# Optimization experiments

Measured on AMD Instinct MI355X. Metric: run time of the kernel, lower is better.

## Reference

```python
import jax, jax.numpy as jnp
import numpy as np
from itertools import product

# Static config
B, H, W, C = 16, 64, 64, 256
WIN = 8            # window size (square)
SHIFT = 4          # cyclic shift
NH = 8             # heads
HD = C // NH       # head dim
N = WIN * WIN      # tokens per window
HIDDEN = 1024


def _rel_pos_index():
    coords = np.stack(np.meshgrid(np.arange(WIN), np.arange(WIN), indexing='ij'))  # (2,w,w)
    flat = coords.reshape(2, -1)                                   # (2,N)
    rel = flat[:, :, None] - flat[:, None, :]                      # (2,N,N)
    rel = rel.transpose(1, 2, 0).astype(np.int64)
    rel[..., 0] += WIN - 1
    rel[..., 1] += WIN - 1
    rel[..., 0] *= 2 * WIN - 1
    return rel.sum(-1)                                             # (N,N)


def _shift_mask():
    # additive mask (nW, N, N) with -100 across shift boundaries (generate_mask)
    img = np.zeros((H, W), dtype=np.float32)
    slices = [(slice(0, -WIN), slice(-WIN, -SHIFT), slice(-SHIFT, None))] * 2
    cnt = 0
    for sx, sy in product(*slices):
        img[sx, sy] = cnt
        cnt += 1
    mw = img.reshape(H // WIN, WIN, W // WIN, WIN).transpose(0, 2, 1, 3).reshape(-1, N)  # (nW,N)
    diff = mw[:, None, :] - mw[:, :, None]
    return np.where(diff != 0, -100.0, 0.0).astype(np.float32)     # (nW,N,N)


REL_IDX = jnp.asarray(_rel_pos_index())
MASK = jnp.asarray(_shift_mask())


def _layernorm(x, scale, bias, eps=1e-5):
    mu = jnp.mean(x, axis=-1, keepdims=True)
    var = jnp.mean(jnp.square(x - mu), axis=-1, keepdims=True)
    return (x - mu) * jax.lax.rsqrt(var + eps) * scale + bias


def setup_inputs() -> dict:
    key = jax.random.key(0)
    ks = jax.random.split(key, 8)
    s = lambda fan_in: 1.0 / np.sqrt(fan_in)
    return {
        'x': jax.random.normal(ks[0], (B, H, W, C), jnp.float32),
        'ln1_scale': jnp.ones((C,), jnp.float32),
        'ln1_bias': jnp.zeros((C,), jnp.float32),
        'qkv_w': jax.random.normal(ks[1], (3 * C, C), jnp.float32) * s(C),
        'qkv_b': jnp.zeros((3 * C,), jnp.float32),
        'proj_w': jax.random.normal(ks[2], (C, C), jnp.float32) * s(C),
        'proj_b': jnp.zeros((C,), jnp.float32),
        'rel_bias': jax.random.normal(ks[3], ((2 * WIN - 1) ** 2, NH), jnp.float32) * 0.02,
        'ln2_scale': jnp.ones((C,), jnp.float32),
        'ln2_bias': jnp.zeros((C,), jnp.float32),
        'mlp_w1': jax.random.normal(ks[4], (HIDDEN, C), jnp.float32) * s(C),
        'mlp_b1': jnp.zeros((HIDDEN,), jnp.float32),
        'mlp_w2': jax.random.normal(ks[5], (C, HIDDEN), jnp.float32) * s(HIDDEN),
        'mlp_b2': jnp.zeros((C,), jnp.float32),
    }


def reference(x, ln1_scale, ln1_bias, qkv_w, qkv_b, proj_w, proj_b, rel_bias,
              ln2_scale, ln2_bias, mlp_w1, mlp_b1, mlp_w2, mlp_b2):
    nWh, nWw = H // WIN, W // WIN
    nW = nWh * nWw

    shortcut = x
    h = _layernorm(x, ln1_scale, ln1_bias)
    # cyclic shift
    h = jnp.roll(h, shift=(-SHIFT, -SHIFT), axis=(1, 2))
    # window partition -> (B*nW, N, C)
    h = h.reshape(B, nWh, WIN, nWw, WIN, C).transpose(0, 1, 3, 2, 4, 5).reshape(B * nW, N, C)

    # qkv
    qkv = h @ qkv_w.T + qkv_b                                # (B*nW, N, 3C)
    qkv = qkv.reshape(B * nW, N, 3, NH, HD)
    q, k, v = qkv[:, :, 0], qkv[:, :, 1], qkv[:, :, 2]       # (B*nW, N, NH, HD)

    scale = 1.0 / np.sqrt(HD)
    attn = jnp.einsum('bnhd,bmhd->bhnm', q * scale, k)       # (B*nW, NH, N, N)
    attn = attn + rel_bias[REL_IDX].transpose(2, 0, 1)[None]  # rel-pos bias (NH,N,N)
    attn = attn.reshape(B, nW, NH, N, N) + MASK[None, :, None]
    attn = jax.nn.softmax(attn.reshape(B * nW, NH, N, N), axis=-1)

    out = jnp.einsum('bhnm,bmhd->bnhd', attn, v).reshape(B * nW, N, C)
    out = out @ proj_w.T + proj_b

    # window reverse + reverse shift
    out = out.reshape(B, nWh, nWw, WIN, WIN, C).transpose(0, 1, 3, 2, 4, 5).reshape(B, H, W, C)
    out = jnp.roll(out, shift=(SHIFT, SHIFT), axis=(1, 2))

    x = shortcut + out
    # MLP
    h2 = _layernorm(x, ln2_scale, ln2_bias)
    h2 = jax.nn.gelu(h2 @ mlp_w1.T + mlp_b1, approximate=False) @ mlp_w2.T + mlp_b2
    return x + h2
```

## Files before the change

### kernel.cpp

```cpp
#include <hip/hip_runtime.h>
#include <hip/hip_bf16.h>
#include <math.h>

#define AS1 __attribute__((address_space(1)))
#define AS3 __attribute__((address_space(3)))

typedef __bf16  bf16x8 __attribute__((ext_vector_type(8)));
typedef float   f32x4  __attribute__((ext_vector_type(4)));
typedef __hip_bfloat16 bf16;

__device__ __forceinline__ void gload_lds16(const void* g, void* l) {
  __builtin_amdgcn_global_load_lds((const AS1 void*)g, (AS3 void*)l, 16, 0, 0);
}

__global__ __launch_bounds__(256) void k_conv_weights(
    const float* __restrict__ qkvw, const float* __restrict__ projw,
    const float* __restrict__ w1, const float* __restrict__ w2,
    bf16* __restrict__ dst)
{
  int i = blockIdx.x * 256 + threadIdx.x;
  float v;
  if (i < 196608)       v = qkvw[i];
  else if (i < 262144)  v = projw[i - 196608];
  else if (i < 524288)  v = w1[i - 262144];
  else                  v = w2[i - 524288];
  dst[i] = __float2bfloat16(v);
}

__global__ __launch_bounds__(256) void k_build_btab(
    const float* __restrict__ rel_bias, float* __restrict__ btab)
{
  int i = blockIdx.x * 256 + threadIdx.x;
  int h = i >> 12, r = i & 4095, n = r >> 6, m = r & 63;
  int idx = ((n >> 3) - (m >> 3) + 7) * 15 + ((n & 7) - (m & 7) + 7);
  btab[i] = rel_bias[idx * 8 + h];
}

__global__ __launch_bounds__(256) void k_ln1_window(
    const float* __restrict__ x, const float* __restrict__ sc,
    const float* __restrict__ bi, bf16* __restrict__ hout)
{
  int t = blockIdx.x * 4 + (threadIdx.x >> 6);
  int lane = threadIdx.x & 63;
  int win = t >> 6, nn = t & 63;
  int b = win >> 6, ww = win & 63;
  int ry = ((ww >> 3) << 3) + (nn >> 3);
  int rx = ((ww & 7) << 3) + (nn & 7);
  int sy = (ry + 4) & 63, sx = (rx + 4) & 63;
  const float* src = x + ((size_t)(((b << 6) + sy) << 6) + sx) * 256;
  f32x4 v = *(const f32x4*)(src + lane * 4);
  float s = v[0] + v[1] + v[2] + v[3];
  #pragma unroll
  for (int o = 1; o < 64; o <<= 1) s += __shfl_xor(s, o);
  float mu = s * (1.0f / 256.0f);
  float d0 = v[0]-mu, d1 = v[1]-mu, d2 = v[2]-mu, d3 = v[3]-mu;
  float q = d0*d0 + d1*d1 + d2*d2 + d3*d3;
  #pragma unroll
  for (int o = 1; o < 64; o <<= 1) q += __shfl_xor(q, o);
  float rstd = rsqrtf(q * (1.0f / 256.0f) + 1e-5f);
  int c = lane * 4;
  union { bf16 h[4]; uint2 u; } pk;
  pk.h[0] = __float2bfloat16(d0 * rstd * sc[c+0] + bi[c+0]);
  pk.h[1] = __float2bfloat16(d1 * rstd * sc[c+1] + bi[c+1]);
  pk.h[2] = __float2bfloat16(d2 * rstd * sc[c+2] + bi[c+2]);
  pk.h[3] = __float2bfloat16(d3 * rstd * sc[c+3] + bi[c+3]);
  *(uint2*)(hout + (size_t)t * 256 + c) = pk.u;
}

template<int EPI>
__global__ __launch_bounds__(256, 2) void k_pipe_ar(
    const bf16* __restrict__ A, const bf16* __restrict__ Bw,
    const float* __restrict__ bias,
    float* __restrict__ Cf, bf16* __restrict__ Cb,
    const float* __restrict__ resid,
    const float* __restrict__ ln2s, const float* __restrict__ ln2b,
    bf16* __restrict__ ln2out, int N)
{
  __shared__ __align__(16) char lds[65536 + 10240];

  const int tid = threadIdx.x;
  const int wid = tid >> 6;
  const int lane = tid & 63;
  const int l15 = lane & 15, lh = lane >> 4;
  const int rowBase = blockIdx.x * 128 + wid * 32;
  const int NC = N >> 5;
  char* scr = lds + 65536 + wid * 2560;

  auto stage = [&](int c) {
    char* dst = lds + (c & 3) * 16384;
    const char* srcB = (const char*)Bw + (size_t)c * 32 * 512;
    #pragma unroll
    for (int i = 0; i < 4; ++i) {
      int off = (i * 256 + tid) * 16;
      int r = off >> 9, cb = off & 511;
      int csw = cb ^ ((r & 7) << 4);
      gload_lds16(srcB + (size_t)r * 512 + csw, dst + off);
    }
  };

  bf16x8 af[2][8];
  {
    const bf16* a0 = A + (size_t)(rowBase + l15) * 256 + lh * 8;
    #pragma unroll
    for (int kk = 0; kk < 8; ++kk) {
      af[0][kk] = *(const bf16x8*)(a0 + kk * 32);
      af[1][kk] = *(const bf16x8*)(a0 + 4096 + kk * 32);
    }
  }

  auto remap = [&](int row) -> size_t {
    int win = row >> 6, nn = row & 63;
    int b = win >> 6, ww = win & 63;
    int ry = ((ww >> 3) << 3) + (nn >> 3);
    int rx = ((ww & 7) << 3) + (nn & 7);
    int fy = (ry + 4) & 63, fx = (rx + 4) & 63;
    return ((size_t)(((b << 6) + fy) << 6) + fx) * 256;
  };
  size_t ra0 = 0, ra1 = 0;
  size_t rbA, rbB;
  if (EPI == 2) {
    ra0 = remap(rowBase + l15);
    ra1 = remap(rowBase + 16 + l15);
    rbA = remap(rowBase + (lane >> 2));
    rbB = remap(rowBase + 16 + (lane >> 2));
  } else {
    rbA = (size_t)(rowBase + (lane >> 2)) * N;
    rbB = rbA + (size_t)16 * N;
  }

  const int cl = lh * 4;
  f32x4 bc0 = *(const f32x4*)(bias + cl);
  f32x4 bc1 = *(const f32x4*)(bias + cl + 16);
  f32x4 rc00, rc10, rc01, rc11;
  if (EPI == 2) {
    rc00 = *(const f32x4*)(resid + ra0 + cl);
    rc10 = *(const f32x4*)(resid + ra1 + cl);
    rc01 = *(const f32x4*)(resid + ra0 + cl + 16);
    rc11 = *(const f32x4*)(resid + ra1 + cl + 16);
  }
  stage(0); stage(1); stage(2);
  asm volatile("s_waitcnt vmcnt(8)" ::: "memory");
  __builtin_amdgcn_sched_barrier(0);

  float s0 = 0.f, q0 = 0.f, s1 = 0.f, q1 = 0.f;

  for (int c = 0; c < NC; ++c) {
    __builtin_amdgcn_s_barrier();
    __builtin_amdgcn_sched_barrier(0);

    f32x4 bn0, bn1, rn00, rn10, rn01, rn11;
    if (c + 1 < NC) {
      const int ncl = (c + 1) * 32 + cl;
      bn0 = *(const f32x4*)(bias + ncl);
      bn1 = *(const f32x4*)(bias + ncl + 16);
      if (EPI == 2) {
        rn00 = *(const f32x4*)(resid + ra0 + ncl);
        rn10 = *(const f32x4*)(resid + ra1 + ncl);
        rn01 = *(const f32x4*)(resid + ra0 + ncl + 16);
        rn11 = *(const f32x4*)(resid + ra1 + ncl + 16);
      }
    }
    if (c + 3 < NC) stage(c + 3);

    const char* buf = lds + (c & 3) * 16384;
    const int xr = (l15 & 7) << 4;
    const int base0 = l15 * 512;
    f32x4 a00 = (f32x4){0.f,0.f,0.f,0.f};
    f32x4 a10 = (f32x4){0.f,0.f,0.f,0.f};
    f32x4 a01 = (f32x4){0.f,0.f,0.f,0.f};
    f32x4 a11 = (f32x4){0.f,0.f,0.f,0.f};
    #pragma unroll
    for (int kk = 0; kk < 8; ++kk) {
      const int ko = (kk * 64 + lh * 16) ^ xr;
      bf16x8 b0 = *(const bf16x8*)(buf + base0 + ko);
      bf16x8 b1 = *(const bf16x8*)(buf + base0 + 8192 + ko);
      a00 = __builtin_amdgcn_mfma_f32_16x16x32_bf16(b0, af[0][kk], a00, 0, 0, 0);
      a10 = __builtin_amdgcn_mfma_f32_16x16x32_bf16(b0, af[1][kk], a10, 0, 0, 0);
      a01 = __builtin_amdgcn_mfma_f32_16x16x32_bf16(b1, af[0][kk], a01, 0, 0, 0);
      a11 = __builtin_amdgcn_mfma_f32_16x16x32_bf16(b1, af[1][kk], a11, 0, 0, 0);
    }

    const int cbs = c * 32 + (lane & 3) * 8;
    if (EPI == 0 || EPI == 1) {
      auto cvt = [](float v) -> bf16 {
        if (EPI == 1) {
          float w = fmaf(v * v, 0.1029434f, 2.3022083f);
          float e = __builtin_amdgcn_exp2f(-v * w);
          v = v * __builtin_amdgcn_rcpf(1.0f + e);
        }
        return __float2bfloat16(v);
      };
      union { bf16 h[4]; uint2 u; } p00, p01, p10, p11;
      #pragma unroll
      for (int j = 0; j < 4; ++j) {
        p00.h[j] = cvt(a00[j] + bc0[j]);
        p01.h[j] = cvt(a01[j] + bc1[j]);
        p10.h[j] = cvt(a10[j] + bc0[j]);
        p11.h[j] = cvt(a11[j] + bc1[j]);
      }
      *(uint2*)(scr + l15 * 80 + lh * 8)            = p00.u;
      *(uint2*)(scr + l15 * 80 + 32 + lh * 8)       = p01.u;
      *(uint2*)(scr + (16 + l15) * 80 + lh * 8)     = p10.u;
      *(uint2*)(scr + (16 + l15) * 80 + 32 + lh * 8)= p11.u;
      uint4 r0 = *(const uint4*)(scr + (lane >> 2) * 80 + (lane & 3) * 16);
      uint4 r1 = *(const uint4*)(scr + (16 + (lane >> 2)) * 80 + (lane & 3) * 16);
      *(uint4*)(Cb + rbA + cbs) = r0;
      *(uint4*)(Cb + rbB + cbs) = r1;
    } else {
      const int colb0 = c * 32 + cl, colb1 = colb0 + 16;
      f32x4 o00, o10, o01, o11;
      #pragma unroll
      for (int j = 0; j < 4; ++j) {
        o00[j] = a00[j] + bc0[j] + rc00[j];
        o10[j] = a10[j] + bc0[j] + rc10[j];
        o01[j] = a01[j] + bc1[j] + rc01[j];
        o11[j] = a11[j] + bc1[j] + rc11[j];
      }
      *(f32x4*)(Cf + ra0 + colb0) = o00;
      *(f32x4*)(Cf + ra1 + colb0) = o10;
      *(f32x4*)(Cf + ra0 + colb1) = o01;
      *(f32x4*)(Cf + ra1 + colb1) = o11;
      #pragma unroll
      for (int j = 0; j < 4; ++j) {
        s0 += o00[j] + o01[j];  q0 += o00[j]*o00[j] + o01[j]*o01[j];
        s1 += o10[j] + o11[j];  q1 += o10[j]*o10[j] + o11[j]*o11[j];
      }
    }

    if (c + 1 < NC) {
      bc0 = bn0; bc1 = bn1;
      if (EPI == 2) { rc00 = rn00; rc10 = rn10; rc01 = rn01; rc11 = rn11; }
    }

    if (c + 1 < NC) {
      if (EPI == 2) {
        if (c == 0)            { asm volatile("s_waitcnt vmcnt(18)" ::: "memory"); }
        else if (c + 3 < NC)   { asm volatile("s_waitcnt vmcnt(28)" ::: "memory"); }
        else                   { asm volatile("s_waitcnt vmcnt(6)"  ::: "memory"); }
      } else {
        if (c == 0)            { asm volatile("s_waitcnt vmcnt(12)" ::: "memory"); }
        else if (c + 3 < NC)   { asm volatile("s_waitcnt vmcnt(16)" ::: "memory"); }
        else                   { asm volatile("s_waitcnt vmcnt(6)"  ::: "memory"); }
      }
      __builtin_amdgcn_sched_barrier(0);
    }
  }

  if (EPI == 2) {
    s0 += __shfl_xor(s0, 16); s0 += __shfl_xor(s0, 32);
    q0 += __shfl_xor(q0, 16); q0 += __shfl_xor(q0, 32);
    s1 += __shfl_xor(s1, 16); s1 += __shfl_xor(s1, 32);
    q1 += __shfl_xor(q1, 16); q1 += __shfl_xor(q1, 32);
    float mu0 = s0 * (1.0f / 256.0f);
    float rs0 = rsqrtf(q0 * (1.0f / 256.0f) - mu0 * mu0 + 1e-5f);
    float mu1 = s1 * (1.0f / 256.0f);
    float rs1 = rsqrtf(q1 * (1.0f / 256.0f) - mu1 * mu1 + 1e-5f);
    for (int c = 0; c < NC; ++c) {
      const int cb0 = c * 32 + cl, cb1 = cb0 + 16;
      f32x4 v00 = *(const f32x4*)(Cf + ra0 + cb0);
      f32x4 v01 = *(const f32x4*)(Cf + ra0 + cb1);
      f32x4 v10 = *(const f32x4*)(Cf + ra1 + cb0);
      f32x4 v11 = *(const f32x4*)(Cf + ra1 + cb1);
      f32x4 sa = *(const f32x4*)(ln2s + cb0);
      f32x4 sb = *(const f32x4*)(ln2s + cb1);
      f32x4 ba = *(const f32x4*)(ln2b + cb0);
      f32x4 bb = *(const f32x4*)(ln2b + cb1);
      union { bf16 h[4]; uint2 u; } p00, p01, p10, p11;
      #pragma unroll
      for (int j = 0; j < 4; ++j) {
        p00.h[j] = __float2bfloat16((v00[j] - mu0) * rs0 * sa[j] + ba[j]);
        p01.h[j] = __float2bfloat16((v01[j] - mu0) * rs0 * sb[j] + bb[j]);
        p10.h[j] = __float2bfloat16((v10[j] - mu1) * rs1 * sa[j] + ba[j]);
        p11.h[j] = __float2bfloat16((v11[j] - mu1) * rs1 * sb[j] + bb[j]);
      }
      *(uint2*)(scr + l15 * 80 + lh * 8)             = p00.u;
      *(uint2*)(scr + l15 * 80 + 32 + lh * 8)        = p01.u;
      *(uint2*)(scr + (16 + l15) * 80 + lh * 8)      = p10.u;
      *(uint2*)(scr + (16 + l15) * 80 + 32 + lh * 8) = p11.u;
      uint4 r0 = *(const uint4*)(scr + (lane >> 2) * 80 + (lane & 3) * 16);
      uint4 r1 = *(const uint4*)(scr + (16 + (lane >> 2)) * 80 + (lane & 3) * 16);
      const int cbs = c * 32 + (lane & 3) * 8;
      *(uint4*)(ln2out + rbA + cbs) = r0;
      *(uint4*)(ln2out + rbB + cbs) = r1;
    }
  }
}

__global__ __launch_bounds__(256, 2) void k_pipe_bt(
    const bf16* __restrict__ A, const bf16* __restrict__ Bw,
    const float* __restrict__ bias, float* __restrict__ Cf)
{
  __shared__ __align__(16) char lds[73728];

  const int tid = threadIdx.x;
  const int wid = tid >> 6;
  const int lane = tid & 63;
  const int l15 = lane & 15, lh = lane >> 4;
  const int wr = (wid >> 1) * 64;
  const int wc = (wid & 1) * 128;
  const int rowBase = blockIdx.x * 128;

  auto stage = [&](int t) {
    char* dA = lds + (t % 3) * 24576;
    char* dB = dA + 8192;
    #pragma unroll
    for (int i = 0; i < 2; ++i) {
      int off = (i * 256 + tid) * 16;
      int r = off >> 6, cb = off & 63;
      int csw = cb ^ ((r & 3) << 4);
      gload_lds16((const char*)(A + (size_t)(rowBase + r) * 1024 + t * 32) + csw, dA + off);
    }
    #pragma unroll
    for (int i = 0; i < 4; ++i) {
      int off = (i * 256 + tid) * 16;
      int r = off >> 6, cb = off & 63;
      int csw = cb ^ ((r & 3) << 4);
      gload_lds16((const char*)(Bw + (size_t)r * 1024 + t * 32) + csw, dB + off);
    }
  };

  f32x4 acc[4][8];
  #pragma unroll
  for (int m = 0; m < 4; ++m)
    #pragma unroll
    for (int n = 0; n < 8; ++n) acc[m][n] = (f32x4){0.f,0.f,0.f,0.f};

  stage(0);
  stage(1);
  asm volatile("s_waitcnt vmcnt(6)" ::: "memory");
  __builtin_amdgcn_sched_barrier(0);

  for (int t = 0; t < 32; ++t) {
    __builtin_amdgcn_s_barrier();
    __builtin_amdgcn_sched_barrier(0);

    if (t + 2 < 32) stage(t + 2);

    const char* bufA = lds + (t % 3) * 24576;
    const char* bufB = bufA + 8192;
    bf16x8 af[4], bfr[8];
    #pragma unroll
    for (int m = 0; m < 4; ++m) {
      int rA = wr + m * 16 + l15;
      af[m] = *(const bf16x8*)(bufA + rA * 64 + ((lh * 16) ^ ((rA & 3) << 4)));
    }
    #pragma unroll
    for (int n = 0; n < 8; ++n) {
      int rB = wc + n * 16 + l15;
      bfr[n] = *(const bf16x8*)(bufB + rB * 64 + ((lh * 16) ^ ((rB & 3) << 4)));
    }
    #pragma unroll
    for (int m = 0; m < 4; ++m)
      #pragma unroll
      for (int n = 0; n < 8; ++n)
        acc[m][n] = __builtin_amdgcn_mfma_f32_16x16x32_bf16(bfr[n], af[m], acc[m][n], 0, 0, 0);

    if (t + 2 < 32) { asm volatile("s_waitcnt vmcnt(6)" ::: "memory"); }
    else if (t < 31) { asm volatile("s_waitcnt vmcnt(0)" ::: "memory"); }
    __builtin_amdgcn_sched_barrier(0);
  }

  #pragma unroll
  for (int m = 0; m < 4; ++m) {
    size_t rowAddr = (size_t)(rowBase + wr + m * 16 + l15) * 256;
    #pragma unroll
    for (int n = 0; n < 8; ++n) {
      const int colb = wc + n * 16 + lh * 4;
      const f32x4 b4 = *(const f32x4*)(bias + colb);
      f32x4* p = (f32x4*)(Cf + rowAddr + colb);
      f32x4 cc = *p;
      #pragma unroll
      for (int j = 0; j < 4; ++j) cc[j] += acc[m][n][j] + b4[j];
      *p = cc;
    }
  }
}

__global__ __launch_bounds__(256) void k_attn(
    const bf16* __restrict__ qkv, const float* __restrict__ btab,
    bf16* __restrict__ outp)
{
  __shared__ __align__(16) char smem[71680];
  float* sb = (float*)smem;
  const int tid = threadIdx.x, wid = tid >> 6, lane = tid & 63;
  const int l15 = lane & 15, lh = lane >> 4;
  const int h = blockIdx.x >> 8;
  const int win = ((blockIdx.x & 255) << 2) + wid;
  const int tb = win << 6;
  char* plw = smem + 16384 + wid * 9216;
  char* vtw = smem + 16384 + 36864 + wid * 4608;

  for (int i = tid; i < 4096; i += 256) sb[i] = btab[(h << 12) + i];
  __syncthreads();

  bf16x8 qf[4], kf[4];
  #pragma unroll
  for (int m = 0; m < 4; ++m) {
    size_t base = (size_t)(tb + m * 16 + l15) * 768 + h * 32 + lh * 8;
    qf[m] = *(const bf16x8*)(qkv + base);
    kf[m] = *(const bf16x8*)(qkv + base + 256);
  }
  f32x4 s[4][4];
  #pragma unroll
  for (int i = 0; i < 4; ++i)
    #pragma unroll
    for (int j = 0; j < 4; ++j) {
      s[i][j] = (f32x4){0.f,0.f,0.f,0.f};
      s[i][j] = __builtin_amdgcn_mfma_f32_16x16x32_bf16(qf[i], kf[j], s[i][j], 0, 0, 0);
    }

  #pragma unroll
  for (int it = 0; it < 32; ++it) {
    int idx = it * 64 + lane;
    int m = idx >> 5, d = idx & 31;
    bf16 vv = qkv[(size_t)(tb + m) * 768 + 512 + h * 32 + d];
    *(bf16*)(vtw + d * 144 + m * 2) = vv;
  }

  int ww = win & 63, wi = ww >> 3, wj = ww & 7;
  int labm[4];
  #pragma unroll
  for (int jf = 0; jf < 4; ++jf) {
    int m = jf * 16 + l15;
    int yy = wi * 8 + (m >> 3), xx = wj * 8 + (m & 7);
    labm[jf] = (yy < 56 ? 0 : (yy < 60 ? 1 : 2)) * 3 + (xx < 56 ? 0 : (xx < 60 ? 1 : 2));
  }
  float rsum[4][4];
  const float scale = 0.17677669529663687f;
  #pragma unroll
  for (int i = 0; i < 4; ++i) {
    #pragma unroll
    for (int j = 0; j < 4; ++j) {
      int n = i * 16 + lh * 4 + j;
      int yy = wi * 8 + (n >> 3), xx = wj * 8 + (n & 7);
      int labn = (yy < 56 ? 0 : (yy < 60 ? 1 : 2)) * 3 + (xx < 56 ? 0 : (xx < 60 ? 1 : 2));
      float vals[4]; float mx = -1e30f;
      #pragma unroll
      for (int jf = 0; jf < 4; ++jf) {
        int m = jf * 16 + l15;
        float v = s[i][jf][j] * scale + sb[(n << 6) + m];
        if (labn != labm[jf]) v -= 100.0f;
        vals[jf] = v; mx = fmaxf(mx, v);
      }
      #pragma unroll
      for (int o = 1; o < 16; o <<= 1) mx = fmaxf(mx, __shfl_xor(mx, o));
      float sum = 0.0f;
      #pragma unroll
      for (int jf = 0; jf < 4; ++jf) {
        float e = __expf(vals[jf] - mx);
        sum += e;
        *(bf16*)(plw + n * 144 + (jf * 16 + l15) * 2) = __float2bfloat16(e);
      }
      #pragma unroll
      for (int o = 1; o < 16; o <<= 1) sum += __shfl_xor(sum, o);
      rsum[i][j] = sum;
    }
  }
  __syncthreads();

  f32x4 o[4][2];
  #pragma unroll
  for (int i = 0; i < 4; ++i) { o[i][0] = (f32x4){0.f,0.f,0.f,0.f}; o[i][1] = (f32x4){0.f,0.f,0.f,0.f}; }
  #pragma unroll
  for (int kk = 0; kk < 2; ++kk) {
    bf16x8 pf[4], vf[2];
    #pragma unroll
    for (int i = 0; i < 4; ++i)
      pf[i] = *(const bf16x8*)(plw + (i * 16 + l15) * 144 + kk * 64 + lh * 16);
    #pragma unroll
    for (int df = 0; df < 2; ++df)
      vf[df] = *(const bf16x8*)(vtw + (df * 16 + l15) * 144 + kk * 64 + lh * 16);
    #pragma unroll
    for (int i = 0; i < 4; ++i)
      #pragma unroll
      for (int df = 0; df < 2; ++df)
        o[i][df] = __builtin_amdgcn_mfma_f32_16x16x32_bf16(pf[i], vf[df], o[i][df], 0, 0, 0);
  }
  #pragma unroll
  for (int i = 0; i < 4; ++i)
    #pragma unroll
    for (int df = 0; df < 2; ++df)
      #pragma unroll
      for (int j = 0; j < 4; ++j) {
        int n = i * 16 + lh * 4 + j;
        int d = df * 16 + l15;
        float v = o[i][df][j] / rsum[i][j];
        outp[(size_t)(tb + n) * 256 + h * 32 + d] = __float2bfloat16(v);
      }
}

extern "C" void kernel_launch(void* const* d_in, const int* in_sizes, int n_in,
                              void* d_out, int out_size, void* d_ws, size_t ws_size,
                              hipStream_t stream) {
  (void)in_sizes; (void)n_in; (void)out_size; (void)ws_size;
  const float* x      = (const float*)d_in[0];
  const float* ln1_s  = (const float*)d_in[1];
  const float* ln1_b  = (const float*)d_in[2];
  const float* qkv_w  = (const float*)d_in[3];
  const float* qkv_b  = (const float*)d_in[4];
  const float* proj_w = (const float*)d_in[5];
  const float* proj_b = (const float*)d_in[6];
  const float* rel_b  = (const float*)d_in[7];
  const float* ln2_s  = (const float*)d_in[8];
  const float* ln2_b  = (const float*)d_in[9];
  const float* w1     = (const float*)d_in[10];
  const float* b1     = (const float*)d_in[11];
  const float* w2     = (const float*)d_in[12];
  const float* b2     = (const float*)d_in[13];

  char* ws = (char*)d_ws;
  bf16*  wqkv  = (bf16*)(ws + 0);
  bf16*  wproj = wqkv + 196608;
  bf16*  wm1   = wqkv + 262144;
  bf16*  wm2   = wqkv + 524288;
  float* btab  = (float*)(ws + 1572864);
  bf16*  hbuf  = (bf16*)(ws + 2097152);
  bf16*  qkvb  = (bf16*)(ws + 35651584);
  bf16*  attnb = (bf16*)(ws + 136314880);
  bf16*  ln2buf = hbuf;
  bf16*  actb  = qkvb;
  float* x1    = (float*)d_out;

  k_conv_weights<<<3072, 256, 0, stream>>>(qkv_w, proj_w, w1, w2, wqkv);
  k_build_btab<<<128, 256, 0, stream>>>(rel_b, btab);
  k_ln1_window<<<16384, 256, 0, stream>>>(x, ln1_s, ln1_b, hbuf);
  k_pipe_ar<0><<<512, 256, 0, stream>>>(hbuf, wqkv, qkv_b, nullptr, qkvb, nullptr,
                                        nullptr, nullptr, nullptr, 768);
  k_attn<<<2048, 256, 0, stream>>>(qkvb, btab, attnb);
  k_pipe_ar<2><<<512, 256, 0, stream>>>(attnb, wproj, proj_b, x1, nullptr, x,
                                        ln2_s, ln2_b, ln2buf, 256);
  k_pipe_ar<1><<<512, 256, 0, stream>>>(ln2buf, wm1, b1, nullptr, actb, nullptr,
                                        nullptr, nullptr, nullptr, 1024);
  k_pipe_bt<<<512, 256, 0, stream>>>(actb, wm2, b2, x1);
}
```

Baseline: 309.4 us.

## Fuse MLP fc1+GELU+fc2 into one kernel keeping hidden activations on-chip

```diff
diff --git a/kernel.cpp b/kernel.cpp
--- a/kernel.cpp
+++ b/kernel.cpp
@@ -181,22 +181,14 @@
     }
 
     const int cbs = c * 32 + (lane & 3) * 8;
-    if (EPI == 0 || EPI == 1) {
-      auto cvt = [](float v) -> bf16 {
-        if (EPI == 1) {
-          float w = fmaf(v * v, 0.1029434f, 2.3022083f);
-          float e = __builtin_amdgcn_exp2f(-v * w);
-          v = v * __builtin_amdgcn_rcpf(1.0f + e);
-        }
-        return __float2bfloat16(v);
-      };
+    if (EPI == 0) {
       union { bf16 h[4]; uint2 u; } p00, p01, p10, p11;
       #pragma unroll
       for (int j = 0; j < 4; ++j) {
-        p00.h[j] = cvt(a00[j] + bc0[j]);
-        p01.h[j] = cvt(a01[j] + bc1[j]);
-        p10.h[j] = cvt(a10[j] + bc0[j]);
-        p11.h[j] = cvt(a11[j] + bc1[j]);
+        p00.h[j] = __float2bfloat16(a00[j] + bc0[j]);
+        p01.h[j] = __float2bfloat16(a01[j] + bc1[j]);
+        p10.h[j] = __float2bfloat16(a10[j] + bc0[j]);
+        p11.h[j] = __float2bfloat16(a11[j] + bc1[j]);
       }
       *(uint2*)(scr + l15 * 80 + lh * 8)            = p00.u;
       *(uint2*)(scr + l15 * 80 + 32 + lh * 8)       = p01.u;
@@ -286,91 +278,132 @@
   }
 }
 
-__global__ __launch_bounds__(256, 2) void k_pipe_bt(
-    const bf16* __restrict__ A, const bf16* __restrict__ Bw,
-    const float* __restrict__ bias, float* __restrict__ Cf)
+__global__ __launch_bounds__(256, 2) void k_mlp(
+    const bf16* __restrict__ A, const bf16* __restrict__ W1,
+    const float* __restrict__ B1, const bf16* __restrict__ W2,
+    const float* __restrict__ B2, float* __restrict__ X1)
 {
-  __shared__ __align__(16) char lds[73728];
+  __shared__ __align__(16) char lds[79872];
 
   const int tid = threadIdx.x;
   const int wid = tid >> 6;
   const int lane = tid & 63;
   const int l15 = lane & 15, lh = lane >> 4;
-  const int wr = (wid >> 1) * 64;
-  const int wc = (wid & 1) * 128;
-  const int rowBase = blockIdx.x * 128;
-
-  auto stage = [&](int t) {
-    char* dA = lds + (t % 3) * 24576;
-    char* dB = dA + 8192;
-    #pragma unroll
-    for (int i = 0; i < 2; ++i) {
-      int off = (i * 256 + tid) * 16;
-      int r = off >> 6, cb = off & 63;
-      int csw = cb ^ ((r & 3) << 4);
-      gload_lds16((const char*)(A + (size_t)(rowBase + r) * 1024 + t * 32) + csw, dA + off);
-    }
+  const int rowBase = blockIdx.x * 128 + wid * 32;
+  char* scr   = lds + 65536 + wid * 2560;
+  char* b1lds = lds + 75776;
+
+  auto stage = [&](int c) {
+    char* slot = lds + (c & 1) * 32768;
+    const char* srcW1 = (const char*)W1 + (size_t)c * 32 * 512;
     #pragma unroll
     for (int i = 0; i < 4; ++i) {
       int off = (i * 256 + tid) * 16;
-      int r = off >> 6, cb = off & 63;
-      int csw = cb ^ ((r & 3) << 4);
-      gload_lds16((const char*)(Bw + (size_t)r * 1024 + t * 32) + csw, dB + off);
+      int r = off >> 9, cb = off & 511;
+      int csw = cb ^ ((r & 7) << 4);
+      gload_lds16(srcW1 + (size_t)r * 512 + csw, slot + off);
+    }
+    #pragma unroll
+    for (int i = 0; i < 4; ++i) {
+      int off = (i * 256 + tid) * 16;
+      int ch = off >> 12, row = (off >> 4) & 255;
+      gload_lds16((const char*)W2 + (size_t)row * 2048 + (size_t)c * 64 + ch * 16,
+                  slot + 16384 + off);
     }
   };
 
-  f32x4 acc[4][8];
-  #pragma unroll
-  for (int m = 0; m < 4; ++m)
-    #pragma unroll
-    for (int n = 0; n < 8; ++n) acc[m][n] = (f32x4){0.f,0.f,0.f,0.f};
-
+  gload_lds16((const char*)B1 + tid * 16, b1lds + tid * 16);
+  bf16x8 af[2][8];
+  {
+    const bf16* a0 = A + (size_t)(rowBase + l15) * 256 + lh * 8;
+    #pragma unroll
+    for (int kk = 0; kk < 8; ++kk) {
+      af[0][kk] = *(const bf16x8*)(a0 + kk * 32);
+      af[1][kk] = *(const bf16x8*)(a0 + 4096 + kk * 32);
+    }
+  }
   stage(0);
-  stage(1);
-  asm volatile("s_waitcnt vmcnt(6)" ::: "memory");
+  asm volatile("s_waitcnt vmcnt(0)" ::: "memory");
   __builtin_amdgcn_sched_barrier(0);
 
-  for (int t = 0; t < 32; ++t) {
+  f32x4 acc2[2][16];
+  #pragma unroll
+  for (int m = 0; m < 2; ++m)
+    #pragma unroll
+    for (int n = 0; n < 16; ++n) acc2[m][n] = (f32x4){0.f,0.f,0.f,0.f};
+
+  for (int c = 0; c < 32; ++c) {
     __builtin_amdgcn_s_barrier();
     __builtin_amdgcn_sched_barrier(0);
 
-    if (t + 2 < 32) stage(t + 2);
-
-    const char* bufA = lds + (t % 3) * 24576;
-    const char* bufB = bufA + 8192;
-    bf16x8 af[4], bfr[8];
-    #pragma unroll
-    for (int m = 0; m < 4; ++m) {
-      int rA = wr + m * 16 + l15;
-      af[m] = *(const bf16x8*)(bufA + rA * 64 + ((lh * 16) ^ ((rA & 3) << 4)));
-    }
-    #pragma unroll
-    for (int n = 0; n < 8; ++n) {
-      int rB = wc + n * 16 + l15;
-      bfr[n] = *(const bf16x8*)(bufB + rB * 64 + ((lh * 16) ^ ((rB & 3) << 4)));
-    }
-    #pragma unroll
-    for (int m = 0; m < 4; ++m)
-      #pragma unroll
-      for (int n = 0; n < 8; ++n)
-        acc[m][n] = __builtin_amdgcn_mfma_f32_16x16x32_bf16(bfr[n], af[m], acc[m][n], 0, 0, 0);
-
-    if (t + 2 < 32) { asm volatile("s_waitcnt vmcnt(6)" ::: "memory"); }
-    else if (t < 31) { asm volatile("s_waitcnt vmcnt(0)" ::: "memory"); }
-    __builtin_amdgcn_sched_barrier(0);
-  }
-
-  #pragma unroll
-  for (int m = 0; m < 4; ++m) {
-    size_t rowAddr = (size_t)(rowBase + wr + m * 16 + l15) * 256;
-    #pragma unroll
-    for (int n = 0; n < 8; ++n) {
-      const int colb = wc + n * 16 + lh * 4;
-      const f32x4 b4 = *(const f32x4*)(bias + colb);
-      f32x4* p = (f32x4*)(Cf + rowAddr + colb);
+    if (c + 1 < 32) stage(c + 1);
+
+    const char* slot = lds + (c & 1) * 32768;
+    const int xr = (l15 & 7) << 4;
+    const int base0 = l15 * 512;
+    f32x4 a00 = (f32x4){0.f,0.f,0.f,0.f};
+    f32x4 a10 = (f32x4){0.f,0.f,0.f,0.f};
+    f32x4 a01 = (f32x4){0.f,0.f,0.f,0.f};
+    f32x4 a11 = (f32x4){0.f,0.f,0.f,0.f};
+    #pragma unroll
+    for (int kk = 0; kk < 8; ++kk) {
+      const int ko = (kk * 64 + lh * 16) ^ xr;
+      bf16x8 b0 = *(const bf16x8*)(slot + base0 + ko);
+      bf16x8 b1 = *(const bf16x8*)(slot + base0 + 8192 + ko);
+      a00 = __builtin_amdgcn_mfma_f32_16x16x32_bf16(b0, af[0][kk], a00, 0, 0, 0);
+      a10 = __builtin_amdgcn_mfma_f32_16x16x32_bf16(b0, af[1][kk], a10, 0, 0, 0);
+      a01 = __builtin_amdgcn_mfma_f32_16x16x32_bf16(b1, af[0][kk], a01, 0, 0, 0);
+      a11 = __builtin_amdgcn_mfma_f32_16x16x32_bf16(b1, af[1][kk], a11, 0, 0, 0);
+    }
+
+    f32x4 bv0 = *(const f32x4*)(b1lds + c * 128 + lh * 16);
+    f32x4 bv1 = *(const f32x4*)(b1lds + c * 128 + 64 + lh * 16);
+    auto gelu = [](float v) -> bf16 {
+      float w = fmaf(v * v, 0.1029434f, 2.3022083f);
+      float e = __builtin_amdgcn_exp2f(-v * w);
+      return __float2bfloat16(v * __builtin_amdgcn_rcpf(1.0f + e));
+    };
+    union { bf16 h[4]; uint2 u; } p00, p01, p10, p11;
+    #pragma unroll
+    for (int j = 0; j < 4; ++j) {
+      p00.h[j] = gelu(a00[j] + bv0[j]);
+      p01.h[j] = gelu(a01[j] + bv1[j]);
+      p10.h[j] = gelu(a10[j] + bv0[j]);
+      p11.h[j] = gelu(a11[j] + bv1[j]);
+    }
+    *(uint2*)(scr + l15 * 80 + lh * 8)             = p00.u;
+    *(uint2*)(scr + l15 * 80 + 32 + lh * 8)        = p01.u;
+    *(uint2*)(scr + (16 + l15) * 80 + lh * 8)      = p10.u;
+    *(uint2*)(scr + (16 + l15) * 80 + 32 + lh * 8) = p11.u;
+    bf16x8 actf0 = *(const bf16x8*)(scr + l15 * 80 + lh * 16);
+    bf16x8 actf1 = *(const bf16x8*)(scr + (16 + l15) * 80 + lh * 16);
+
+    const char* w2buf = slot + 16384;
+    const int w2k = lh * 4096;
+    #pragma unroll
+    for (int n = 0; n < 16; ++n) {
+      bf16x8 wf = *(const bf16x8*)(w2buf + w2k + (n * 16 + l15) * 16);
+      acc2[0][n] = __builtin_amdgcn_mfma_f32_16x16x32_bf16(wf, actf0, acc2[0][n], 0, 0, 0);
+      acc2[1][n] = __builtin_amdgcn_mfma_f32_16x16x32_bf16(wf, actf1, acc2[1][n], 0, 0, 0);
+    }
+
+    if (c + 1 < 32) {
+      asm volatile("s_waitcnt vmcnt(0)" ::: "memory");
+      __builtin_amdgcn_sched_barrier(0);
+    }
+  }
+
+  #pragma unroll
+  for (int m = 0; m < 2; ++m) {
+    size_t rowAddr = (size_t)(rowBase + m * 16 + l15) * 256;
+    #pragma unroll
+    for (int n = 0; n < 16; ++n) {
+      const int colb = n * 16 + lh * 4;
+      const f32x4 b4 = *(const f32x4*)(B2 + colb);
+      f32x4* p = (f32x4*)(X1 + rowAddr + colb);
       f32x4 cc = *p;
       #pragma unroll
-      for (int j = 0; j < 4; ++j) cc[j] += acc[m][n][j] + b4[j];
+      for (int j = 0; j < 4; ++j) cc[j] += acc2[m][n][j] + b4[j];
       *p = cc;
     }
   }
@@ -518,7 +551,6 @@
   bf16*  qkvb  = (bf16*)(ws + 35651584);
   bf16*  attnb = (bf16*)(ws + 136314880);
   bf16*  ln2buf = hbuf;
-  bf16*  actb  = qkvb;
   float* x1    = (float*)d_out;
 
   k_conv_weights<<<3072, 256, 0, stream>>>(qkv_w, proj_w, w1, w2, wqkv);
@@ -529,7 +561,5 @@
   k_attn<<<2048, 256, 0, stream>>>(qkvb, btab, attnb);
   k_pipe_ar<2><<<512, 256, 0, stream>>>(attnb, wproj, proj_b, x1, nullptr, x,
                                         ln2_s, ln2_b, ln2buf, 256);
-  k_pipe_ar<1><<<512, 256, 0, stream>>>(ln2buf, wm1, b1, nullptr, actb, nullptr,
-                                        nullptr, nullptr, nullptr, 1024);
-  k_pipe_bt<<<512, 256, 0, stream>>>(actb, wm2, b2, x1);
-}
+  k_mlp<<<512, 256, 0, stream>>>(ln2buf, wm1, b1, wm2, b2, x1);
+}
```

New measurement: 275.5 us. 11.0% less time.
